# Kernel tuning notes

Hardware: AMD Instinct MI355X
Metric: run time of the kernel (lower is better)

## Reference

```python
import jax, jax.numpy as jnp
import numpy as np

N = 80000        # nodes
E = 1280000      # edges (avg degree 16)
D_IN, H1, H2, D_OUT = 64, 64, 64, 64


def _glorot(key, fan_in, fan_out):
    s = np.sqrt(6.0 / (fan_in + fan_out)).astype(np.float32)
    return jax.random.uniform(key, (fan_in, fan_out), jnp.float32, -s, s)


def setup_inputs() -> dict:
    key = jax.random.key(0)
    ks = jax.random.split(key, 5)
    X = jax.random.normal(ks[0], (N, D_IN), jnp.float32)
    edge_index = jax.random.randint(ks[1], (2, E), 0, N, dtype=jnp.int32).astype(jnp.int64)
    W1 = _glorot(ks[2], D_IN, H1)
    W2 = _glorot(ks[3], H1, H2)
    W3 = _glorot(ks[4], H2, D_OUT)
    b1 = jnp.zeros((H1,), jnp.float32)
    b2 = jnp.zeros((H2,), jnp.float32)
    b3 = jnp.zeros((D_OUT,), jnp.float32)
    return {"X": X, "edge_index": edge_index,
            "W1": W1, "b1": b1, "W2": W2, "b2": b2, "W3": W3, "b3": b3}


def _gcn_conv(x, W, b, src, dst, n):
    """PyG GCNConv: symmetric-normalized mean over A + I, then linear + bias.
    x' = D^{-1/2} (A + I) D^{-1/2} (x W) + b, deg counts self-loops."""
    x = x @ W                                   # [N, F_out]
    # in-degree including self loop (edge weights are 1)
    deg = jnp.ones((n,), x.dtype).at[dst].add(1.0)
    dinv = jax.lax.rsqrt(deg)                   # deg >= 1 always
    coef = dinv[src] * dinv[dst]                # [E]
    msg = x[src] * coef[:, None]                # [E, F_out] gather
    agg = jnp.zeros_like(x).at[dst].add(msg)    # scatter-add to targets
    agg = agg + x * (dinv * dinv)[:, None]      # self-loop contribution
    return agg + b


def reference(X, edge_index, W1, b1, W2, b2, W3, b3):
    src, dst = edge_index[0], edge_index[1]
    n = X.shape[0]
    h = jax.nn.relu(_gcn_conv(X, W1, b1, src, dst, n))
    h = jax.nn.relu(_gcn_conv(h, W2, b2, src, dst, n))
    out = _gcn_conv(h, W3, b3, src, dst, n)     # no activation on last layer
    return out
```

## Files before the change

### kernel.cpp

```cpp
#include <hip/hip_runtime.h>
#include <hip/hip_fp16.h>

#define NN 80000
#define NE 1280000
#define F  64
#define BSH 9
#define NB  157
#define CAP 12288
#define EPB 5120
#define EPT 20
#define PBLK (NE / EPB)

typedef _Float16 half_t;
typedef _Float16 half8 __attribute__((ext_vector_type(8)));
typedef float f32x4 __attribute__((ext_vector_type(4)));
typedef unsigned int uint_t;

__device__ __forceinline__ float2 h2f2(uint_t u) {
    __half2 h = *(__half2*)&u;
    return __half22float2(h);
}

__global__ void detect_idx64(const int* __restrict__ idx, int* __restrict__ flag,
                             int* __restrict__ bcur) {
    __shared__ int allzero;
    if (threadIdx.x == 0) allzero = 1;
    __syncthreads();
    if (idx[2 * threadIdx.x + 1] != 0) allzero = 0;
    if (threadIdx.x < NB) bcur[threadIdx.x] = 0;
    __syncthreads();
    if (threadIdx.x == 0) *flag = allzero;
}

__device__ __forceinline__ int ld_src(const int* __restrict__ idx, int e, int is64) {
    return is64 ? idx[2 * e] : idx[e];
}
__device__ __forceinline__ int ld_dst(const int* __restrict__ idx, int e, int is64) {
    return is64 ? idx[2 * NE + 2 * e] : idx[NE + e];
}

__global__ __launch_bounds__(256) void partition_kernel(
        const int* __restrict__ idx, const int* __restrict__ flag,
        int* __restrict__ bcur, int* __restrict__ ebuf) {
    __shared__ int cnt[NB];
    __shared__ int lbase[NB];
    __shared__ int gbase[NB];
    __shared__ int lds_val[EPB];
    __shared__ int lds_gaddr[EPB];
    int tid = threadIdx.x;
    for (int i = tid; i < NB; i += 256) cnt[i] = 0;
    __syncthreads();
    int is64 = *flag;
    int e0 = blockIdx.x * EPB;
    int val[EPT], br[EPT];
    #pragma unroll
    for (int j = 0; j < EPT; ++j) {
        int e = e0 + j * 256 + tid;
        int s = ld_src(idx, e, is64);
        int d = ld_dst(idx, e, is64);
        int b = d >> BSH;
        val[j] = ((d & ((1 << BSH) - 1)) << 17) | s;
        int r = atomicAdd(&cnt[b], 1);
        br[j] = (b << 13) | r;
    }
    __syncthreads();
    if (tid < 64) {
        int carry = 0;
        for (int base = 0; base < NB; base += 64) {
            int i2 = base + tid;
            int v = (i2 < NB) ? cnt[i2] : 0;
            int incl = v;
            #pragma unroll
            for (int d2 = 1; d2 < 64; d2 <<= 1) {
                int t = __shfl_up(incl, d2, 64);
                if (tid >= d2) incl += t;
            }
            if (i2 < NB) lbase[i2] = carry + incl - v;
            carry += __shfl(incl, 63);
        }
    } else if (tid - 64 < NB) {
        int b = tid - 64;
        gbase[b] = atomicAdd(&bcur[b], cnt[b]);
    }
    __syncthreads();
    #pragma unroll
    for (int j = 0; j < EPT; ++j) {
        int b = br[j] >> 13, r = br[j] & 8191;
        int slot = lbase[b] + r;
        int g = gbase[b] + r;
        lds_val[slot]   = val[j];
        lds_gaddr[slot] = (g < CAP) ? (b * CAP + g) : -1;
    }
    __syncthreads();
    for (int i = tid; i < EPB; i += 256) {
        int a = lds_gaddr[i];
        if (a >= 0) ebuf[a] = lds_val[i];
    }
}

__global__ __launch_bounds__(256) void bucket_sort_kernel(
        const int* __restrict__ bcur, const int* __restrict__ ebuf,
        int* __restrict__ edata, int* __restrict__ row_ptr,
        float* __restrict__ dinv) {
    __shared__ int cnt[512];
    __shared__ int off[512];
    __shared__ int lds_out[CAP];
    __shared__ int ebase_s;
    int b = blockIdx.x, tid = threadIdx.x;
    cnt[tid] = 0; cnt[tid + 256] = 0;
    if (tid < 64) {
        int carry = 0;
        for (int base = 0; base < NB; base += 64) {
            int i2 = base + tid;
            int v = (i2 < NB) ? min(bcur[i2], CAP) : 0;
            int incl = v;
            #pragma unroll
            for (int d2 = 1; d2 < 64; d2 <<= 1) {
                int t = __shfl_up(incl, d2, 64);
                if (tid >= d2) incl += t;
            }
            if (i2 == b) ebase_s = carry + incl - v;
            carry += __shfl(incl, 63);
        }
    }
    __syncthreads();
    int bcnt = min(bcur[b], CAP);
    int ebase = ebase_s;
    const int* src = ebuf + b * CAP;
    for (int i = tid; i < bcnt; i += 256)
        atomicAdd(&cnt[src[i] >> 17], 1);
    __syncthreads();
    if (tid < 64) {
        int carry = 0;
        #pragma unroll
        for (int base = 0; base < 512; base += 64) {
            int v = cnt[base + tid];
            int incl = v;
            #pragma unroll
            for (int d2 = 1; d2 < 64; d2 <<= 1) {
                int t = __shfl_up(incl, d2, 64);
                if (tid >= d2) incl += t;
            }
            off[base + tid] = carry + incl - v;
            carry += __shfl(incl, 63);
        }
    }
    __syncthreads();
    int n0 = b << BSH;
    for (int i = tid; i < 512; i += 256) {
        int n = n0 + i;
        if (n < NN) {
            row_ptr[n] = ebase + off[i];
            dinv[n] = rsqrtf((float)cnt[i] + 1.f);
        } else if (n == NN) {
            row_ptr[NN] = ebase + off[i];
        }
    }
    __syncthreads();
    for (int i = tid; i < bcnt; i += 256) {
        int w = src[i];
        int pos = atomicAdd(&off[w >> 17], 1);
        lds_out[pos] = w & 0x1FFFF;
    }
    __syncthreads();
    for (int i = tid; i < bcnt; i += 256)
        edata[ebase + i] = lds_out[i];
}

__global__ void prescale_kernel(const float* __restrict__ x, const float* __restrict__ dinv,
                                half_t* __restrict__ y) {
    int tid = blockIdx.x * blockDim.x + threadIdx.x;
    if (tid >= NN * 16) return;
    int n = tid >> 4, q = tid & 15;
    float c = dinv[n];
    float4 v = ((const float4*)(x + (size_t)n * F))[q];
    half_t h[4] = { (half_t)(v.x * c), (half_t)(v.y * c),
                    (half_t)(v.z * c), (half_t)(v.w * c) };
    ((uint2*)(y + (size_t)n * F))[q] = *(uint2*)h;
}

__global__ __launch_bounds__(256) void gather_kernel(const half_t* __restrict__ y,
        const int* __restrict__ edata, const int* __restrict__ row_ptr,
        const float* __restrict__ dinv, half_t* __restrict__ agg) {
    int n = blockIdx.x * 4 + (threadIdx.x >> 6);
    int lane = threadIdx.x & 63;
    int sub = lane >> 4, fl = lane & 15;
    int p0 = row_ptr[n], p1 = row_ptr[n + 1];
    float a0 = 0.f, a1 = 0.f, a2 = 0.f, a3 = 0.f;
    for (int base = p0; base < p1; base += 32) {
        int s[8]; float m[8];
        #pragma unroll
        for (int j = 0; j < 8; ++j) {
            int q = base + j * 4 + sub;
            int qc = q < p1 ? q : p1 - 1;
            s[j] = edata[qc];
            m[j] = (q < p1) ? 1.f : 0.f;
        }
        uint2 u[8];
        #pragma unroll
        for (int j = 0; j < 8; ++j)
            u[j] = ((const uint2*)(y + (size_t)s[j] * F))[fl];
        #pragma unroll
        for (int j = 0; j < 8; ++j) {
            float2 lo = h2f2(u[j].x), hi = h2f2(u[j].y);
            a0 = fmaf(m[j], lo.x, a0);
            a1 = fmaf(m[j], lo.y, a1);
            a2 = fmaf(m[j], hi.x, a2);
            a3 = fmaf(m[j], hi.y, a3);
        }
    }
    a0 += __shfl_down(a0, 32); a1 += __shfl_down(a1, 32);
    a2 += __shfl_down(a2, 32); a3 += __shfl_down(a3, 32);
    a0 += __shfl_down(a0, 16); a1 += __shfl_down(a1, 16);
    a2 += __shfl_down(a2, 16); a3 += __shfl_down(a3, 16);
    if (sub == 0) {
        float dv = dinv[n];
        uint2 us = ((const uint2*)(y + (size_t)n * F))[fl];
        float2 slo = h2f2(us.x), shi = h2f2(us.y);
        half_t h[4] = { (half_t)(dv * (a0 + slo.x)), (half_t)(dv * (a1 + slo.y)),
                        (half_t)(dv * (a2 + shi.x)), (half_t)(dv * (a3 + shi.y)) };
        ((uint2*)(agg + (size_t)n * F))[fl] = *(uint2*)h;
    }
}

template <int RELU, int SCALE, int LAST>
__global__ __launch_bounds__(256) void gemm_mfma(
        const half_t* __restrict__ A, const float* __restrict__ W,
        const float* __restrict__ bias, const float* __restrict__ dinv,
        half_t* __restrict__ out_h, float* __restrict__ out_f32) {
    __shared__ half_t Wt[64][72];
    __shared__ half_t xt[128][72];
    int tid = threadIdx.x;
    for (int i = tid; i < 4096; i += 256) {
        int k = i >> 6, n2 = i & 63;
        Wt[n2][k] = (half_t)W[i];
    }
    int n0 = blockIdx.x * 128;
    for (int i2 = tid; i2 < 2048; i2 += 256) {
        int r = i2 >> 4, c = i2 & 15;
        ((uint2*)&xt[r][0])[c] = ((const uint2*)(A + (size_t)(n0 + r) * F))[c];
    }
    __syncthreads();
    int wv = tid >> 6, lane = tid & 63;
    int m = lane & 15, q = lane >> 4;
    #pragma unroll
    for (int rt = 0; rt < 2; ++rt) {
        int rbase = wv * 32 + rt * 16;
        const half_t* arow = &xt[rbase + m][q * 8];
        half8 A0 = *(const half8*)arow;
        half8 A1 = *(const half8*)(arow + 32);
        #pragma unroll
        for (int ct = 0; ct < 4; ++ct) {
            const half_t* brow = &Wt[ct * 16 + m][q * 8];
            half8 B0 = *(const half8*)brow;
            half8 B1 = *(const half8*)(brow + 32);
            f32x4 c = {0.f, 0.f, 0.f, 0.f};
            c = __builtin_amdgcn_mfma_f32_16x16x32_f16(A0, B0, c, 0, 0, 0);
            c = __builtin_amdgcn_mfma_f32_16x16x32_f16(A1, B1, c, 0, 0, 0);
            float bv = bias[ct * 16 + m];
            #pragma unroll
            for (int r = 0; r < 4; ++r) {
                int row = n0 + rbase + q * 4 + r;
                float v = c[r] + bv;
                if (RELU) v = fmaxf(v, 0.f);
                if (SCALE) v *= dinv[row];
                int col = ct * 16 + m;
                if (LAST) out_f32[(size_t)row * F + col] = v;
                else      out_h[(size_t)row * F + col] = (half_t)v;
            }
        }
    }
}

extern "C" void kernel_launch(void* const* d_in, const int* in_sizes, int n_in,
                              void* d_out, int out_size, void* d_ws, size_t ws_size,
                              hipStream_t stream) {
    const float* X  = (const float*)d_in[0];
    const int*  idx = (const int*)d_in[1];
    const float* W1 = (const float*)d_in[2];
    const float* b1 = (const float*)d_in[3];
    const float* W2 = (const float*)d_in[4];
    const float* b2 = (const float*)d_in[5];
    const float* W3 = (const float*)d_in[6];
    const float* b3 = (const float*)d_in[7];
    float* out = (float*)d_out;

    char* ws = (char*)d_ws;
    int*    flag    = (int*)(ws + 0);
    int*    bcur    = (int*)(ws + 256);
    int*    row_ptr = (int*)(ws + 1024);
    float*  dinv    = (float*)(ws + 321280);
    int*    edata   = (int*)(ws + 641536);
    half_t* ybufA   = (half_t*)(ws + 5761536);
    half_t* ybufB   = (half_t*)(ws + 16001536);
    int*    ebuf    = (int*)(ws + 26241536);

    detect_idx64<<<1, 1024, 0, stream>>>(idx, flag, bcur);
    partition_kernel<<<PBLK, 256, 0, stream>>>(idx, flag, bcur, ebuf);
    bucket_sort_kernel<<<NB, 256, 0, stream>>>(bcur, ebuf, edata, row_ptr, dinv);
    prescale_kernel<<<(NN * 16) / 256, 256, 0, stream>>>(X, dinv, ybufA);

    const int gBlocks = NN / 4;
    const int mBlocks = NN / 128;

    gather_kernel<<<gBlocks, 256, 0, stream>>>(ybufA, edata, row_ptr, dinv, ybufB);
    gemm_mfma<1, 1, 0><<<mBlocks, 256, 0, stream>>>(ybufB, W1, b1, dinv, ybufA, nullptr);
    gather_kernel<<<gBlocks, 256, 0, stream>>>(ybufA, edata, row_ptr, dinv, ybufB);
    gemm_mfma<1, 1, 0><<<mBlocks, 256, 0, stream>>>(ybufB, W2, b2, dinv, ybufA, nullptr);
    gather_kernel<<<gBlocks, 256, 0, stream>>>(ybufA, edata, row_ptr, dinv, ybufB);
    gemm_mfma<0, 0, 1><<<mBlocks, 256, 0, stream>>>(ybufB, W3, b3, dinv, nullptr, out);
}
```

Before: 250.6 us.

## Fuse prescale into bucket sort, drop detect kernel, recompute dinv in gather

Removes the separate detect_idx64 kernel: each partition block now checks int64 layout itself, and bcur is zeroed with a memset. The X prescale is folded into bucket_sort_kernel, which now runs with 512 threads per block. Partition blocks shrink to 2560 edges, giving more blocks. Gather recomputes dinv from the row_ptr difference instead of loading it. This cuts launches and one pass over the data, but the fused prescale runs on only 157 blocks, which may limit its bandwidth.

```diff
diff --git a/kernel.cpp b/kernel.cpp
--- a/kernel.cpp
+++ b/kernel.cpp
@@ -7,8 +7,8 @@
 #define BSH 9
 #define NB  157
 #define CAP 12288
-#define EPB 5120
-#define EPT 20
+#define EPB 2560
+#define EPT 10
 #define PBLK (NE / EPB)
 
 typedef _Float16 half_t;
@@ -21,17 +21,6 @@
     return __half22float2(h);
 }
 
-__global__ void detect_idx64(const int* __restrict__ idx, int* __restrict__ flag,
-                             int* __restrict__ bcur) {
-    __shared__ int allzero;
-    if (threadIdx.x == 0) allzero = 1;
-    __syncthreads();
-    if (idx[2 * threadIdx.x + 1] != 0) allzero = 0;
-    if (threadIdx.x < NB) bcur[threadIdx.x] = 0;
-    __syncthreads();
-    if (threadIdx.x == 0) *flag = allzero;
-}
-
 __device__ __forceinline__ int ld_src(const int* __restrict__ idx, int e, int is64) {
     return is64 ? idx[2 * e] : idx[e];
 }
@@ -40,17 +29,21 @@
 }
 
 __global__ __launch_bounds__(256) void partition_kernel(
-        const int* __restrict__ idx, const int* __restrict__ flag,
+        const int* __restrict__ idx,
         int* __restrict__ bcur, int* __restrict__ ebuf) {
     __shared__ int cnt[NB];
     __shared__ int lbase[NB];
     __shared__ int gbase[NB];
     __shared__ int lds_val[EPB];
     __shared__ int lds_gaddr[EPB];
+    __shared__ int is64_s;
     int tid = threadIdx.x;
+    if (tid == 0) is64_s = 1;
     for (int i = tid; i < NB; i += 256) cnt[i] = 0;
     __syncthreads();
-    int is64 = *flag;
+    if (idx[2 * tid + 1] != 0) is64_s = 0;
+    __syncthreads();
+    int is64 = is64_s;
     int e0 = blockIdx.x * EPB;
     int val[EPT], br[EPT];
     #pragma unroll
@@ -98,16 +91,17 @@
     }
 }
 
-__global__ __launch_bounds__(256) void bucket_sort_kernel(
+__global__ __launch_bounds__(512) void bucket_sort_kernel(
         const int* __restrict__ bcur, const int* __restrict__ ebuf,
+        const float* __restrict__ X,
         int* __restrict__ edata, int* __restrict__ row_ptr,
-        float* __restrict__ dinv) {
+        float* __restrict__ dinv, half_t* __restrict__ y0) {
     __shared__ int cnt[512];
     __shared__ int off[512];
     __shared__ int lds_out[CAP];
     __shared__ int ebase_s;
     int b = blockIdx.x, tid = threadIdx.x;
-    cnt[tid] = 0; cnt[tid + 256] = 0;
+    cnt[tid] = 0;
     if (tid < 64) {
         int carry = 0;
         for (int base = 0; base < NB; base += 64) {
@@ -127,7 +121,7 @@
     int bcnt = min(bcur[b], CAP);
     int ebase = ebase_s;
     const int* src = ebuf + b * CAP;
-    for (int i = tid; i < bcnt; i += 256)
+    for (int i = tid; i < bcnt; i += 512)
         atomicAdd(&cnt[src[i] >> 17], 1);
     __syncthreads();
     if (tid < 64) {
@@ -147,41 +141,39 @@
     }
     __syncthreads();
     int n0 = b << BSH;
-    for (int i = tid; i < 512; i += 256) {
+    {
+        int n = n0 + tid;
+        if (n < NN) {
+            row_ptr[n] = ebase + off[tid];
+            dinv[n] = rsqrtf((float)cnt[tid] + 1.f);
+        } else if (n == NN) {
+            row_ptr[NN] = ebase + off[tid];
+        }
+    }
+    __syncthreads();
+    for (int j = tid; j < 512 * 16; j += 512) {
+        int i = j >> 4, q = j & 15;
         int n = n0 + i;
-        if (n < NN) {
-            row_ptr[n] = ebase + off[i];
-            dinv[n] = rsqrtf((float)cnt[i] + 1.f);
-        } else if (n == NN) {
-            row_ptr[NN] = ebase + off[i];
-        }
-    }
-    __syncthreads();
-    for (int i = tid; i < bcnt; i += 256) {
+        if (n >= NN) break;
+        float dv = rsqrtf((float)cnt[i] + 1.f);
+        float4 v = ((const float4*)(X + (size_t)n * F))[q];
+        half_t h[4] = { (half_t)(v.x * dv), (half_t)(v.y * dv),
+                        (half_t)(v.z * dv), (half_t)(v.w * dv) };
+        ((uint2*)(y0 + (size_t)n * F))[q] = *(uint2*)h;
+    }
+    for (int i = tid; i < bcnt; i += 512) {
         int w = src[i];
         int pos = atomicAdd(&off[w >> 17], 1);
         lds_out[pos] = w & 0x1FFFF;
     }
     __syncthreads();
-    for (int i = tid; i < bcnt; i += 256)
+    for (int i = tid; i < bcnt; i += 512)
         edata[ebase + i] = lds_out[i];
-}
-
-__global__ void prescale_kernel(const float* __restrict__ x, const float* __restrict__ dinv,
-                                half_t* __restrict__ y) {
-    int tid = blockIdx.x * blockDim.x + threadIdx.x;
-    if (tid >= NN * 16) return;
-    int n = tid >> 4, q = tid & 15;
-    float c = dinv[n];
-    float4 v = ((const float4*)(x + (size_t)n * F))[q];
-    half_t h[4] = { (half_t)(v.x * c), (half_t)(v.y * c),
-                    (half_t)(v.z * c), (half_t)(v.w * c) };
-    ((uint2*)(y + (size_t)n * F))[q] = *(uint2*)h;
 }
 
 __global__ __launch_bounds__(256) void gather_kernel(const half_t* __restrict__ y,
         const int* __restrict__ edata, const int* __restrict__ row_ptr,
-        const float* __restrict__ dinv, half_t* __restrict__ agg) {
+        half_t* __restrict__ agg) {
     int n = blockIdx.x * 4 + (threadIdx.x >> 6);
     int lane = threadIdx.x & 63;
     int sub = lane >> 4, fl = lane & 15;
@@ -214,7 +206,7 @@
     a0 += __shfl_down(a0, 16); a1 += __shfl_down(a1, 16);
     a2 += __shfl_down(a2, 16); a3 += __shfl_down(a3, 16);
     if (sub == 0) {
-        float dv = dinv[n];
+        float dv = rsqrtf((float)(p1 - p0) + 1.f);
         uint2 us = ((const uint2*)(y + (size_t)n * F))[fl];
         float2 slo = h2f2(us.x), shi = h2f2(us.y);
         half_t h[4] = { (half_t)(dv * (a0 + slo.x)), (half_t)(dv * (a1 + slo.y)),
@@ -286,7 +278,6 @@
     float* out = (float*)d_out;
 
     char* ws = (char*)d_ws;
-    int*    flag    = (int*)(ws + 0);
     int*    bcur    = (int*)(ws + 256);
     int*    row_ptr = (int*)(ws + 1024);
     float*  dinv    = (float*)(ws + 321280);
@@ -295,18 +286,18 @@
     half_t* ybufB   = (half_t*)(ws + 16001536);
     int*    ebuf    = (int*)(ws + 26241536);
 
-    detect_idx64<<<1, 1024, 0, stream>>>(idx, flag, bcur);
-    partition_kernel<<<PBLK, 256, 0, stream>>>(idx, flag, bcur, ebuf);
-    bucket_sort_kernel<<<NB, 256, 0, stream>>>(bcur, ebuf, edata, row_ptr, dinv);
-    prescale_kernel<<<(NN * 16) / 256, 256, 0, stream>>>(X, dinv, ybufA);
+    hipMemsetAsync(bcur, 0, NB * sizeof(int), stream);
+    partition_kernel<<<PBLK, 256, 0, stream>>>(idx, bcur, ebuf);
+    bucket_sort_kernel<<<NB, 512, 0, stream>>>(bcur, ebuf, X, edata, row_ptr,
+                                               dinv, ybufA);
 
     const int gBlocks = NN / 4;
     const int mBlocks = NN / 128;
 
-    gather_kernel<<<gBlocks, 256, 0, stream>>>(ybufA, edata, row_ptr, dinv, ybufB);
+    gather_kernel<<<gBlocks, 256, 0, stream>>>(ybufA, edata, row_ptr, ybufB);
     gemm_mfma<1, 1, 0><<<mBlocks, 256, 0, stream>>>(ybufB, W1, b1, dinv, ybufA, nullptr);
-    gather_kernel<<<gBlocks, 256, 0, stream>>>(ybufA, edata, row_ptr, dinv, ybufB);
+    gather_kernel<<<gBlocks, 256, 0, stream>>>(ybufA, edata, row_ptr, ybufB);
     gemm_mfma<1, 1, 0><<<mBlocks, 256, 0, stream>>>(ybufB, W2, b2, dinv, ybufA, nullptr);
-    gather_kernel<<<gBlocks, 256, 0, stream>>>(ybufA, edata, row_ptr, dinv, ybufB);
+    gather_kernel<<<gBlocks, 256, 0, stream>>>(ybufA, edata, row_ptr, ybufB);
     gemm_mfma<0, 0, 1><<<mBlocks, 256, 0, stream>>>(ybufB, W3, b3, dinv, nullptr, out);
 }
```

Measured after the change: 257.1 us. +2.6%, slower.
